# Kernel tuning notes

Measured on AMD Instinct MI355X. Metric: run time of the kernel, lower is better.

## Reference

```python
import jax, jax.numpy as jnp
import numpy as np

N_NODES = 100000
N_EDGES = 1600000
IN_CH = 64
HID = 64
OUT_CH = 128
EDGE_CH = 3
OBS_RANGE = 0.5
ATK_RANGE = 0.3


def setup_inputs() -> dict:
    key = jax.random.key(0)
    k = jax.random.split(key, 8)
    # node features: first column is an integer node type in {0,1,2}
    node_type = jax.random.randint(k[0], (N_NODES, 1), 0, 3).astype(jnp.float32)
    feats = jax.random.normal(k[1], (N_NODES, IN_CH - 1), dtype=jnp.float32)
    x = jnp.concatenate([node_type, feats], axis=-1)
    edge_index = jax.random.randint(k[2], (2, N_EDGES), 0, N_NODES)
    # edge_attr[:,0] = distance in [0,1)
    edge_attr = jax.random.uniform(k[3], (N_EDGES, EDGE_CH), dtype=jnp.float32)
    s1 = 1.0 / np.sqrt(2 * IN_CH + EDGE_CH)
    s2 = 1.0 / np.sqrt(HID)
    W1 = jax.random.normal(k[4], (2 * IN_CH + EDGE_CH, HID), dtype=jnp.float32) * s1
    b1 = jnp.zeros((HID,), dtype=jnp.float32)
    W2 = jax.random.normal(k[5], (HID, OUT_CH), dtype=jnp.float32) * s2
    b2 = jnp.zeros((OUT_CH,), dtype=jnp.float32)
    return {"x": x, "edge_index": edge_index, "edge_attr": edge_attr,
            "W1": W1, "b1": b1, "W2": W2, "b2": b2}


def reference(x, edge_index, edge_attr, W1, b1, W2, b2):
    src = edge_index[0]  # j (source)
    dst = edge_index[1]  # i (target)
    x_j = x[src]         # [E, IN_CH]
    x_i = x[dst]         # [E, IN_CH]
    h = jnp.concatenate([x_i, x_j, edge_attr], axis=-1)  # [E, 2*IN_CH+3]
    msg = jax.nn.relu(h @ W1 + b1) @ W2 + b2             # [E, OUT_CH]
    dist = edge_attr[:, 0]
    ntype = x_j[:, 0]
    mask = jnp.where(ntype == 0, dist < OBS_RANGE,
                     jnp.where(ntype == 1, dist < ATK_RANGE, True))
    msg = mask[:, None].astype(msg.dtype) * msg
    out = jax.ops.segment_sum(msg, dst, num_segments=x.shape[0])  # [N, OUT_CH]
    return jax.nn.relu(out)
```

## Files before the change

### kernel.cpp

```cpp
#include <hip/hip_runtime.h>

#define N_NODES 100000
#define N_EDGES 1600000
#define IN_CH   64
#define HID_CH  64
#define OUT_CH  128
#define TILE    128
#define N_TILES (N_EDGES / TILE)

typedef __attribute__((ext_vector_type(8))) __bf16    bf16x8;
typedef __attribute__((ext_vector_type(4))) float     f32x4;
typedef __attribute__((ext_vector_type(2))) _Float16  f16x2;
typedef __attribute__((ext_vector_type(8))) _Float16  f16x8;

__device__ __forceinline__ unsigned short f2bf(float f) {
    union { float f; unsigned int i; } c;
    c.f = f;
    unsigned int u = c.i;
    unsigned int r = (u + 0x7FFFu + ((u >> 16) & 1u)) >> 16;
    return (unsigned short)r;
}

__device__ __forceinline__ void atomic_pk_add_f16(unsigned int* addr, f16x2 val) {
    typedef __attribute__((address_space(1))) f16x2 gf16x2;
    __builtin_amdgcn_global_atomic_fadd_v2f16((gf16x2*)(void*)addr, val);
}

__global__ void gnn_prep(const float* __restrict__ xf,
                         unsigned short* __restrict__ xb,
                         unsigned char* __restrict__ ntype,
                         uint4* __restrict__ hz,
                         float4* __restrict__ cz) {
    int i = blockIdx.x * blockDim.x + threadIdx.x;
    if (i < 1600000) {
        float4 v = reinterpret_cast<const float4*>(xf)[i];
        ushort4 o;
        o.x = f2bf(v.x); o.y = f2bf(v.y); o.z = f2bf(v.z); o.w = f2bf(v.w);
        reinterpret_cast<ushort4*>(xb)[i] = o;
        if ((i & 15) == 0) {
            int n = i >> 4;
            ntype[n] = (v.x == 0.0f) ? 0 : ((v.x == 1.0f) ? 1 : 2);
        }
    } else if (i < 2400000) {
        hz[i - 1600000] = (uint4){0u, 0u, 0u, 0u};
    } else if (i < 2425000) {
        cz[i - 2400000] = (float4){0.f, 0.f, 0.f, 0.f};
    }
}

__global__ __launch_bounds__(256, 4) void gnn_edge_hidden(
    const unsigned char*  __restrict__ ntype,
    const unsigned short* __restrict__ xb,
    const int*            __restrict__ eidx,
    const float*          __restrict__ ea,
    const float*          __restrict__ W1,
    const float*          __restrict__ b1,
    unsigned int*         __restrict__ hsum,
    float*                __restrict__ cnt)
{
    __shared__ __align__(16) unsigned short W1T[64][136];
    __shared__ float eas[128][3];
    __shared__ int   dstm[128];
    __shared__ int   srcs[128];

    const int tid  = threadIdx.x;
    const int wave = tid >> 6;
    const int lane = tid & 63;
    const int q    = lane >> 4;
    const int m16  = lane & 15;

    for (int idx = tid; idx < 128 * 64; idx += 256) {
        int k = idx >> 6, n = idx & 63;
        W1T[n][k] = f2bf(W1[idx]);
    }
    if (tid < 64) {
        float4 tl;
        tl.x = W1[128 * 64 + tid];
        tl.y = W1[129 * 64 + tid];
        tl.z = W1[130 * 64 + tid];
        tl.w = b1[tid];
        *reinterpret_cast<float4*>(&W1T[tid][128]) = tl;
    }

    for (int t = blockIdx.x; t < N_TILES; t += gridDim.x) {
        __syncthreads();
        if (tid < 128) {
            int e = t * TILE + tid;
            int s = eidx[e];
            int d = eidx[N_EDGES + e];
            float a0 = ea[e * 3 + 0];
            float a1 = ea[e * 3 + 1];
            float a2 = ea[e * 3 + 2];
            eas[tid][0] = a0; eas[tid][1] = a1; eas[tid][2] = a2;
            int ntc = ntype[s];
            bool mk = (ntc == 0) ? (a0 < 0.5f) : ((ntc == 1) ? (a0 < 0.3f) : true);
            dstm[tid] = mk ? (int)(0x80000000u | (unsigned)d) : 0;
            srcs[tid] = mk ? s : 0;
            if (mk) unsafeAtomicAdd(&cnt[d], 1.0f);
        }
        __syncthreads();

        const int ebase = wave * 32;

        f32x4 acc1[2][4];
#pragma unroll
        for (int mt = 0; mt < 2; ++mt) {
            float e0[4], e1[4], e2[4];
#pragma unroll
            for (int r = 0; r < 4; ++r) {
                int el = ebase + mt * 16 + q * 4 + r;
                e0[r] = eas[el][0]; e1[r] = eas[el][1]; e2[r] = eas[el][2];
            }
#pragma unroll
            for (int nt = 0; nt < 4; ++nt) {
                int n = nt * 16 + m16;
                float4 wt = *reinterpret_cast<const float4*>(&W1T[n][128]);
#pragma unroll
                for (int r = 0; r < 4; ++r)
                    acc1[mt][nt][r] = wt.w + e0[r] * wt.x + e1[r] * wt.y + e2[r] * wt.z;
            }
        }

#pragma unroll
        for (int kc = 0; kc < 4; ++kc) {
            bf16x8 af[2];
#pragma unroll
            for (int mt = 0; mt < 2; ++mt) {
                int el = ebase + mt * 16 + m16;
                int dm = dstm[el];
                int node = (kc < 2) ? (dm & 0x7FFFFFFF) : srcs[el];
                af[mt] = *reinterpret_cast<const bf16x8*>(
                    xb + (size_t)node * IN_CH + (kc & 1) * 32 + q * 8);
            }
#pragma unroll
            for (int nt = 0; nt < 4; ++nt) {
                bf16x8 bfr = *reinterpret_cast<const bf16x8*>(
                    &W1T[nt * 16 + m16][kc * 32 + q * 8]);
                acc1[0][nt] = __builtin_amdgcn_mfma_f32_16x16x32_bf16(af[0], bfr, acc1[0][nt], 0, 0, 0);
                acc1[1][nt] = __builtin_amdgcn_mfma_f32_16x16x32_bf16(af[1], bfr, acc1[1][nt], 0, 0, 0);
            }
        }

#pragma unroll
        for (int mt = 0; mt < 2; ++mt) {
#pragma unroll
            for (int r = 0; r < 4; ++r) {
                int el = ebase + mt * 16 + q * 4 + r;
                int dm = dstm[el];
                if (dm < 0) {
                    unsigned int* hbase = hsum + (size_t)(dm & 0x7FFFFFFF) * 32;
                    float v0 = acc1[mt][0][r]; v0 = v0 > 0.f ? v0 : 0.f;
                    float v1 = acc1[mt][1][r]; v1 = v1 > 0.f ? v1 : 0.f;
                    float v2 = acc1[mt][2][r]; v2 = v2 > 0.f ? v2 : 0.f;
                    float v3 = acc1[mt][3][r]; v3 = v3 > 0.f ? v3 : 0.f;
                    if (v0 + v1 > 0.f) {
                        f16x2 p01 = {(_Float16)v0, (_Float16)v1};
                        atomic_pk_add_f16(hbase + m16, p01);
                    }
                    if (v2 + v3 > 0.f) {
                        f16x2 p23 = {(_Float16)v2, (_Float16)v3};
                        atomic_pk_add_f16(hbase + 16 + m16, p23);
                    }
                }
            }
        }
    }
}

__global__ __launch_bounds__(256, 4) void gnn_node_out(
    const _Float16* __restrict__ hsum,
    const float*    __restrict__ cnt,
    const float*    __restrict__ W2,
    const float*    __restrict__ b2,
    float*          __restrict__ out)
{
    __shared__ __align__(16) unsigned short W2T[128][72];
    __shared__ float b2s[128];

    const int tid  = threadIdx.x;
    const int wave = tid >> 6;
    const int lane = tid & 63;
    const int q    = lane >> 4;
    const int m16  = lane & 15;

    const int nodeBase = (blockIdx.x * 4 + wave) * 32;

    f16x8 hpre[2][2];
    float cc[2][4];
#pragma unroll
    for (int kc = 0; kc < 2; ++kc)
#pragma unroll
        for (int mt = 0; mt < 2; ++mt) {
            int node = nodeBase + mt * 16 + m16;
            if (node >= N_NODES) node = N_NODES - 1;
            hpre[kc][mt] = *reinterpret_cast<const f16x8*>(
                hsum + (size_t)node * HID_CH + kc * 32 + q * 8);
        }
#pragma unroll
    for (int mt = 0; mt < 2; ++mt)
#pragma unroll
        for (int r = 0; r < 4; ++r) {
            int n = nodeBase + mt * 16 + q * 4 + r;
            cc[mt][r] = (n < N_NODES) ? cnt[n] : 0.0f;
        }

    for (int idx = tid; idx < 64 * 128; idx += 256) {
        int p = idx >> 7, n = idx & 127;
        int ch = (p >> 1) + 16 * (p & 1) + ((p >= 32) ? 16 : 0);
        W2T[n][p] = f2bf(W2[ch * 128 + n]);
    }
    if (tid < 128) b2s[tid] = b2[tid];
    __syncthreads();

    if (nodeBase >= N_NODES) return;

    f32x4 acc[2][8];
#pragma unroll
    for (int mt = 0; mt < 2; ++mt)
#pragma unroll
        for (int nt = 0; nt < 8; ++nt)
            acc[mt][nt] = (f32x4){0.0f, 0.0f, 0.0f, 0.0f};

#pragma unroll
    for (int kc = 0; kc < 2; ++kc) {
        bf16x8 af[2];
#pragma unroll
        for (int mt = 0; mt < 2; ++mt) {
            union { bf16x8 v; unsigned short u[8]; } rr;
#pragma unroll
            for (int j = 0; j < 8; ++j) rr.u[j] = f2bf((float)hpre[kc][mt][j]);
            af[mt] = rr.v;
        }
#pragma unroll
        for (int nt = 0; nt < 8; ++nt) {
            bf16x8 bfr = *reinterpret_cast<const bf16x8*>(
                &W2T[nt * 16 + m16][kc * 32 + q * 8]);
            acc[0][nt] = __builtin_amdgcn_mfma_f32_16x16x32_bf16(af[0], bfr, acc[0][nt], 0, 0, 0);
            acc[1][nt] = __builtin_amdgcn_mfma_f32_16x16x32_bf16(af[1], bfr, acc[1][nt], 0, 0, 0);
        }
    }

#pragma unroll
    for (int mt = 0; mt < 2; ++mt) {
        int nn[4];
#pragma unroll
        for (int r = 0; r < 4; ++r)
            nn[r] = nodeBase + mt * 16 + q * 4 + r;
#pragma unroll
        for (int nt = 0; nt < 8; ++nt) {
            int col = nt * 16 + m16;
            float bb = b2s[col];
#pragma unroll
            for (int r = 0; r < 4; ++r) {
                if (nn[r] < N_NODES) {
                    float v = acc[mt][nt][r] + cc[mt][r] * bb;
                    out[(size_t)nn[r] * OUT_CH + col] = v > 0.0f ? v : 0.0f;
                }
            }
        }
    }
}

extern "C" void kernel_launch(void* const* d_in, const int* in_sizes, int n_in,
                              void* d_out, int out_size, void* d_ws, size_t ws_size,
                              hipStream_t stream) {
    const float* x  = (const float*)d_in[0];
    const int*   ei = (const int*)d_in[1];
    const float* ea = (const float*)d_in[2];
    const float* W1 = (const float*)d_in[3];
    const float* b1 = (const float*)d_in[4];
    const float* W2 = (const float*)d_in[5];
    const float* b2 = (const float*)d_in[6];
    float* out = (float*)d_out;

    char* wsb = (char*)d_ws;
    unsigned int*   hsum  = (unsigned int*)wsb;
    float*          cnt   = (float*)(wsb + 12800000);
    unsigned short* xb    = (unsigned short*)(wsb + 13200000);
    unsigned char*  ntype = (unsigned char*)(wsb + 26000000);

    gnn_prep<<<(2425000 + 255) / 256, 256, 0, stream>>>(
        x, xb, ntype, (uint4*)hsum, (float4*)cnt);

    gnn_edge_hidden<<<2048, 256, 0, stream>>>(ntype, xb, ei, ea, W1, b1, hsum, cnt);

    gnn_node_out<<<(N_NODES + 127) / 128, 256, 0, stream>>>(
        (const _Float16*)hsum, cnt, W2, b2, out);
}
```

Before: 271.9 us.

## Sort masked edges by destination via CSR build and reduce in shared memory

Replaces the global fp16 packed atomics on the hidden sum with a counting sort of masked edges by destination: a histogram, a three-kernel scan, and a scatter into packed edge records. Each block then handles 64 destination nodes, accumulates hidden activations in a shared-memory float buffer with run-length merged LDS atomics, and writes hsum once. This removes global atomic contention and the zeroing of hsum, and accumulates in fp32 before the fp16 store. In exchange it adds several launches, an extra pass over the edges, a scatter with global atomics, and 25.6 MB of record traffic. The W2 permutation in the node kernel is simplified to match the new hsum channel layout.

```diff
diff --git a/kernel.cpp b/kernel.cpp
--- a/kernel.cpp
+++ b/kernel.cpp
@@ -6,12 +6,24 @@
 #define HID_CH  64
 #define OUT_CH  128
 #define TILE    128
-#define N_TILES (N_EDGES / TILE)
+#define DPB     64
+#define N_EBLK  ((N_NODES + DPB - 1) / DPB)
+#define N_SCANB ((N_NODES + 255) / 256)
 
 typedef __attribute__((ext_vector_type(8))) __bf16    bf16x8;
 typedef __attribute__((ext_vector_type(4))) float     f32x4;
 typedef __attribute__((ext_vector_type(2))) _Float16  f16x2;
 typedef __attribute__((ext_vector_type(8))) _Float16  f16x8;
+
+#define OFF_HSUM   0
+#define OFF_XB     12800000
+#define OFF_SREC   25600000
+#define OFF_CNT    51200000
+#define OFF_DEG    51600000
+#define OFF_RPTR   52000000
+#define OFF_CUR    52400016
+#define OFF_BSUM   52800016
+#define OFF_NTYPE  52801600
 
 __device__ __forceinline__ unsigned short f2bf(float f) {
     union { float f; unsigned int i; } c;
@@ -21,16 +33,14 @@
     return (unsigned short)r;
 }
 
-__device__ __forceinline__ void atomic_pk_add_f16(unsigned int* addr, f16x2 val) {
-    typedef __attribute__((address_space(1))) f16x2 gf16x2;
-    __builtin_amdgcn_global_atomic_fadd_v2f16((gf16x2*)(void*)addr, val);
+__device__ __forceinline__ bool edge_mask(int ntc, float a0) {
+    return (ntc == 0) ? (a0 < 0.5f) : ((ntc == 1) ? (a0 < 0.3f) : true);
 }
 
 __global__ void gnn_prep(const float* __restrict__ xf,
                          unsigned short* __restrict__ xb,
                          unsigned char* __restrict__ ntype,
-                         uint4* __restrict__ hz,
-                         float4* __restrict__ cz) {
+                         uint4* __restrict__ degz) {
     int i = blockIdx.x * blockDim.x + threadIdx.x;
     if (i < 1600000) {
         float4 v = reinterpret_cast<const float4*>(xf)[i];
@@ -41,27 +51,116 @@
             int n = i >> 4;
             ntype[n] = (v.x == 0.0f) ? 0 : ((v.x == 1.0f) ? 1 : 2);
         }
-    } else if (i < 2400000) {
-        hz[i - 1600000] = (uint4){0u, 0u, 0u, 0u};
-    } else if (i < 2425000) {
-        cz[i - 2400000] = (float4){0.f, 0.f, 0.f, 0.f};
-    }
-}
-
-__global__ __launch_bounds__(256, 4) void gnn_edge_hidden(
-    const unsigned char*  __restrict__ ntype,
+    } else if (i < 1625000) {
+        degz[i - 1600000] = (uint4){0u, 0u, 0u, 0u};
+    }
+}
+
+__global__ void gnn_hist(const int* __restrict__ eidx,
+                         const float* __restrict__ ea,
+                         const unsigned char* __restrict__ ntype,
+                         unsigned int* __restrict__ deg) {
+    int e = blockIdx.x * blockDim.x + threadIdx.x;
+    if (e < N_EDGES) {
+        int s = eidx[e];
+        float a0 = ea[e * 3];
+        if (edge_mask(ntype[s], a0))
+            atomicAdd(deg + eidx[N_EDGES + e], 1u);
+    }
+}
+
+__global__ void gnn_scan_a(const unsigned int* __restrict__ deg,
+                           unsigned int* __restrict__ rptr,
+                           unsigned int* __restrict__ bsum,
+                           float* __restrict__ cnt) {
+    __shared__ unsigned int sd[256];
+    int t = threadIdx.x;
+    int i = blockIdx.x * 256 + t;
+    unsigned v = (i < N_NODES) ? deg[i] : 0u;
+    sd[t] = v;
+    __syncthreads();
+    for (int off = 1; off < 256; off <<= 1) {
+        unsigned x = (t >= off) ? sd[t - off] : 0u;
+        __syncthreads();
+        sd[t] += x;
+        __syncthreads();
+    }
+    unsigned incl = sd[t];
+    if (i < N_NODES) {
+        rptr[i] = incl - v;
+        cnt[i]  = (float)v;
+    }
+    if (t == 255) bsum[blockIdx.x] = incl;
+}
+
+__global__ void gnn_scan_b(unsigned int* __restrict__ bsum,
+                           unsigned int* __restrict__ rptr) {
+    __shared__ unsigned int sd[512];
+    int t = threadIdx.x;
+    unsigned v = (t < N_SCANB) ? bsum[t] : 0u;
+    sd[t] = v;
+    __syncthreads();
+    for (int off = 1; off < 512; off <<= 1) {
+        unsigned x = (t >= off) ? sd[t - off] : 0u;
+        __syncthreads();
+        sd[t] += x;
+        __syncthreads();
+    }
+    if (t < N_SCANB) bsum[t] = sd[t] - v;
+    if (t == 511) rptr[N_NODES] = sd[511];
+}
+
+__global__ void gnn_scan_c(unsigned int* __restrict__ rptr,
+                           const unsigned int* __restrict__ bsum,
+                           unsigned int* __restrict__ cur) {
+    int i = blockIdx.x * 256 + threadIdx.x;
+    if (i < N_NODES) {
+        unsigned r = rptr[i] + bsum[blockIdx.x];
+        rptr[i] = r;
+        cur[i]  = r;
+    }
+}
+
+__global__ void gnn_scatter(const int* __restrict__ eidx,
+                            const float* __restrict__ ea,
+                            const unsigned char* __restrict__ ntype,
+                            unsigned int* __restrict__ cur,
+                            float4* __restrict__ srec) {
+    int e = blockIdx.x * blockDim.x + threadIdx.x;
+    if (e < N_EDGES) {
+        int s = eidx[e];
+        float a0 = ea[e * 3 + 0];
+        if (edge_mask(ntype[s], a0)) {
+            int d = eidx[N_EDGES + e];
+            float a1 = ea[e * 3 + 1];
+            float a2 = ea[e * 3 + 2];
+            unsigned pos = atomicAdd(cur + d, 1u);
+            union { f16x2 v; float f; } pk;
+            pk.v = (f16x2){(_Float16)a1, (_Float16)a2};
+            float4 rec;
+            rec.x = __int_as_float(s);
+            rec.y = __int_as_float(d);
+            rec.z = a0;
+            rec.w = pk.f;
+            srec[pos] = rec;
+        }
+    }
+}
+
+__global__ __launch_bounds__(256, 4) void gnn_edge_sorted(
     const unsigned short* __restrict__ xb,
-    const int*            __restrict__ eidx,
-    const float*          __restrict__ ea,
+    const float4*         __restrict__ srec,
+    const unsigned int*   __restrict__ rptr,
     const float*          __restrict__ W1,
     const float*          __restrict__ b1,
-    unsigned int*         __restrict__ hsum,
-    float*                __restrict__ cnt)
+    unsigned int*         __restrict__ hsum)
 {
     __shared__ __align__(16) unsigned short W1T[64][136];
+    __shared__ float accum[65][64];
     __shared__ float eas[128][3];
-    __shared__ int   dstm[128];
     __shared__ int   srcs[128];
+    __shared__ int   dstg[128];
+    __shared__ int   dstl[128];
 
     const int tid  = threadIdx.x;
     const int wave = tid >> 6;
@@ -81,26 +180,35 @@
         tl.w = b1[tid];
         *reinterpret_cast<float4*>(&W1T[tid][128]) = tl;
     }
-
-    for (int t = blockIdx.x; t < N_TILES; t += gridDim.x) {
-        __syncthreads();
-        if (tid < 128) {
-            int e = t * TILE + tid;
-            int s = eidx[e];
-            int d = eidx[N_EDGES + e];
-            float a0 = ea[e * 3 + 0];
-            float a1 = ea[e * 3 + 1];
-            float a2 = ea[e * 3 + 2];
-            eas[tid][0] = a0; eas[tid][1] = a1; eas[tid][2] = a2;
-            int ntc = ntype[s];
-            bool mk = (ntc == 0) ? (a0 < 0.5f) : ((ntc == 1) ? (a0 < 0.3f) : true);
-            dstm[tid] = mk ? (int)(0x80000000u | (unsigned)d) : 0;
-            srcs[tid] = mk ? s : 0;
-            if (mk) unsafeAtomicAdd(&cnt[d], 1.0f);
-        }
-        __syncthreads();
-
-        const int ebase = wave * 32;
+    for (int idx = tid; idx < 65 * 64; idx += 256)
+        (&accum[0][0])[idx] = 0.0f;
+
+    const int base = blockIdx.x * DPB;
+    const int dEnd = (base + DPB < N_NODES) ? base + DPB : N_NODES;
+    const unsigned eStart = rptr[base];
+    const unsigned eEnd   = rptr[dEnd];
+    __syncthreads();
+
+    const int ebase = wave * 32;
+
+    for (unsigned t0 = eStart; t0 < eEnd; t0 += TILE) {
+        int cntE = (int)(eEnd - t0); if (cntE > TILE) cntE = TILE;
+        if (tid < TILE) {
+            if (tid < cntE) {
+                float4 rec = srec[t0 + tid];
+                int s = __float_as_int(rec.x);
+                int d = __float_as_int(rec.y);
+                srcs[tid] = s; dstg[tid] = d; dstl[tid] = d - base;
+                union { float f; f16x2 v; } pk; pk.f = rec.w;
+                eas[tid][0] = rec.z;
+                eas[tid][1] = (float)pk.v[0];
+                eas[tid][2] = (float)pk.v[1];
+            } else {
+                srcs[tid] = 0; dstg[tid] = 0; dstl[tid] = 64;
+                eas[tid][0] = 0.f; eas[tid][1] = 0.f; eas[tid][2] = 0.f;
+            }
+        }
+        __syncthreads();
 
         f32x4 acc1[2][4];
 #pragma unroll
@@ -127,8 +235,7 @@
 #pragma unroll
             for (int mt = 0; mt < 2; ++mt) {
                 int el = ebase + mt * 16 + m16;
-                int dm = dstm[el];
-                int node = (kc < 2) ? (dm & 0x7FFFFFFF) : srcs[el];
+                int node = (kc < 2) ? dstg[el] : srcs[el];
                 af[mt] = *reinterpret_cast<const bf16x8*>(
                     xb + (size_t)node * IN_CH + (kc & 1) * 32 + q * 8);
             }
@@ -143,26 +250,36 @@
 
 #pragma unroll
         for (int mt = 0; mt < 2; ++mt) {
-#pragma unroll
-            for (int r = 0; r < 4; ++r) {
-                int el = ebase + mt * 16 + q * 4 + r;
-                int dm = dstm[el];
-                if (dm < 0) {
-                    unsigned int* hbase = hsum + (size_t)(dm & 0x7FFFFFFF) * 32;
-                    float v0 = acc1[mt][0][r]; v0 = v0 > 0.f ? v0 : 0.f;
-                    float v1 = acc1[mt][1][r]; v1 = v1 > 0.f ? v1 : 0.f;
-                    float v2 = acc1[mt][2][r]; v2 = v2 > 0.f ? v2 : 0.f;
-                    float v3 = acc1[mt][3][r]; v3 = v3 > 0.f ? v3 : 0.f;
-                    if (v0 + v1 > 0.f) {
-                        f16x2 p01 = {(_Float16)v0, (_Float16)v1};
-                        atomic_pk_add_f16(hbase + m16, p01);
-                    }
-                    if (v2 + v3 > 0.f) {
-                        f16x2 p23 = {(_Float16)v2, (_Float16)v3};
-                        atomic_pk_add_f16(hbase + 16 + m16, p23);
-                    }
-                }
-            }
+            int rowb = ebase + mt * 16 + q * 4;
+            int d0 = dstl[rowb + 0];
+            int d1 = dstl[rowb + 1];
+            int d2 = dstl[rowb + 2];
+            int d3 = dstl[rowb + 3];
+#pragma unroll
+            for (int nt = 0; nt < 4; ++nt) {
+                int ch = nt * 16 + m16;
+                float v0 = acc1[mt][nt][0]; v0 = v0 > 0.f ? v0 : 0.f;
+                float v1 = acc1[mt][nt][1]; v1 = v1 > 0.f ? v1 : 0.f;
+                float v2 = acc1[mt][nt][2]; v2 = v2 > 0.f ? v2 : 0.f;
+                float v3 = acc1[mt][nt][3]; v3 = v3 > 0.f ? v3 : 0.f;
+                float s = v0; int cur = d0;
+                if (d1 == cur) s += v1; else { atomicAdd(&accum[cur][ch], s); s = v1; cur = d1; }
+                if (d2 == cur) s += v2; else { atomicAdd(&accum[cur][ch], s); s = v2; cur = d2; }
+                if (d3 == cur) s += v3; else { atomicAdd(&accum[cur][ch], s); s = v3; cur = d3; }
+                atomicAdd(&accum[cur][ch], s);
+            }
+        }
+        __syncthreads();
+    }
+
+    for (int idx = tid; idx < DPB * 32; idx += 256) {
+        int d = idx >> 5;
+        int c = idx & 31;
+        int gd = base + d;
+        if (gd < N_NODES) {
+            union { f16x2 v; unsigned u; } pk;
+            pk.v = (f16x2){(_Float16)accum[d][2 * c], (_Float16)accum[d][2 * c + 1]};
+            hsum[(size_t)gd * 32 + c] = pk.u;
         }
     }
 }
@@ -205,9 +322,8 @@
         }
 
     for (int idx = tid; idx < 64 * 128; idx += 256) {
-        int p = idx >> 7, n = idx & 127;
-        int ch = (p >> 1) + 16 * (p & 1) + ((p >= 32) ? 16 : 0);
-        W2T[n][p] = f2bf(W2[ch * 128 + n]);
+        int k = idx >> 7, n = idx & 127;
+        W2T[n][k] = f2bf(W2[k * 128 + n]);
     }
     if (tid < 128) b2s[tid] = b2[tid];
     __syncthreads();
@@ -274,16 +390,23 @@
     float* out = (float*)d_out;
 
     char* wsb = (char*)d_ws;
-    unsigned int*   hsum  = (unsigned int*)wsb;
-    float*          cnt   = (float*)(wsb + 12800000);
-    unsigned short* xb    = (unsigned short*)(wsb + 13200000);
-    unsigned char*  ntype = (unsigned char*)(wsb + 26000000);
-
-    gnn_prep<<<(2425000 + 255) / 256, 256, 0, stream>>>(
-        x, xb, ntype, (uint4*)hsum, (float4*)cnt);
-
-    gnn_edge_hidden<<<2048, 256, 0, stream>>>(ntype, xb, ei, ea, W1, b1, hsum, cnt);
-
+    unsigned int*   hsum  = (unsigned int*)  (wsb + OFF_HSUM);
+    unsigned short* xb    = (unsigned short*)(wsb + OFF_XB);
+    float4*         srec  = (float4*)        (wsb + OFF_SREC);
+    float*          cnt   = (float*)         (wsb + OFF_CNT);
+    unsigned int*   deg   = (unsigned int*)  (wsb + OFF_DEG);
+    unsigned int*   rptr  = (unsigned int*)  (wsb + OFF_RPTR);
+    unsigned int*   curp  = (unsigned int*)  (wsb + OFF_CUR);
+    unsigned int*   bsum  = (unsigned int*)  (wsb + OFF_BSUM);
+    unsigned char*  ntype = (unsigned char*) (wsb + OFF_NTYPE);
+
+    gnn_prep<<<(1625000 + 255) / 256, 256, 0, stream>>>(x, xb, ntype, (uint4*)deg);
+    gnn_hist<<<N_EDGES / 256, 256, 0, stream>>>(ei, ea, ntype, deg);
+    gnn_scan_a<<<N_SCANB, 256, 0, stream>>>(deg, rptr, bsum, cnt);
+    gnn_scan_b<<<1, 512, 0, stream>>>(bsum, rptr);
+    gnn_scan_c<<<N_SCANB, 256, 0, stream>>>(rptr, bsum, curp);
+    gnn_scatter<<<N_EDGES / 256, 256, 0, stream>>>(ei, ea, ntype, curp, srec);
+    gnn_edge_sorted<<<N_EBLK, 256, 0, stream>>>(xb, srec, rptr, W1, b1, hsum);
     gnn_node_out<<<(N_NODES + 127) / 128, 256, 0, stream>>>(
         (const _Float16*)hsum, cnt, W2, b2, out);
 }
```

New measurement: 369.6 us. 1.36x slower.

## Precompute per-node W1 projections and reduce edge stage to gather-add-relu

Applied to the files above, without the earlier changes.

Splits the first-layer GEMM by linearity: a new node-level kernel computes x@W1_dst and x@W1_src once per node into an fp16 buffer z. The per-edge kernel then only gathers two 64-channel rows of z, adds the edge-attribute and bias term, applies relu and scatters with packed fp16 atomics, using four threads per edge. Masked edges are skipped early, before the destination and the other attributes are loaded. This removes per-edge MFMA work and x gathers in exchange for an extra 25.6MB z buffer with its write and random reads. It also adds fp16 rounding of the pre-activation and changes the hsum channel ordering, so W2T is now transposed without the previous permutation.

```diff
diff --git a/kernel.cpp b/kernel.cpp
--- a/kernel.cpp
+++ b/kernel.cpp
@@ -5,13 +5,17 @@
 #define IN_CH   64
 #define HID_CH  64
 #define OUT_CH  128
-#define TILE    128
-#define N_TILES (N_EDGES / TILE)
 
 typedef __attribute__((ext_vector_type(8))) __bf16    bf16x8;
 typedef __attribute__((ext_vector_type(4))) float     f32x4;
 typedef __attribute__((ext_vector_type(2))) _Float16  f16x2;
 typedef __attribute__((ext_vector_type(8))) _Float16  f16x8;
+
+#define OFF_HSUM   0
+#define OFF_XB     12800000
+#define OFF_Z      25600000
+#define OFF_CNT    51200000
+#define OFF_NTYPE  51600000
 
 __device__ __forceinline__ unsigned short f2bf(float f) {
     union { float f; unsigned int i; } c;
@@ -48,20 +52,12 @@
     }
 }
 
-__global__ __launch_bounds__(256, 4) void gnn_edge_hidden(
-    const unsigned char*  __restrict__ ntype,
+__global__ __launch_bounds__(256, 4) void gnn_zgemm(
     const unsigned short* __restrict__ xb,
-    const int*            __restrict__ eidx,
-    const float*          __restrict__ ea,
     const float*          __restrict__ W1,
-    const float*          __restrict__ b1,
-    unsigned int*         __restrict__ hsum,
-    float*                __restrict__ cnt)
+    _Float16*             __restrict__ z)
 {
-    __shared__ __align__(16) unsigned short W1T[64][136];
-    __shared__ float eas[128][3];
-    __shared__ int   dstm[128];
-    __shared__ int   srcs[128];
+    __shared__ __align__(16) unsigned short BT[128][72];
 
     const int tid  = threadIdx.x;
     const int wave = tid >> 6;
@@ -69,98 +65,120 @@
     const int q    = lane >> 4;
     const int m16  = lane & 15;
 
-    for (int idx = tid; idx < 128 * 64; idx += 256) {
-        int k = idx >> 6, n = idx & 63;
-        W1T[n][k] = f2bf(W1[idx]);
-    }
+    for (int idx = tid; idx < 64 * 128; idx += 256) {
+        int k = idx >> 7, j = idx & 127;
+        BT[j][k] = f2bf(W1[(k + ((j >= 64) ? 64 : 0)) * 64 + (j & 63)]);
+    }
+    __syncthreads();
+
+    const int nodeBase = (blockIdx.x * 4 + wave) * 32;
+    if (nodeBase >= N_NODES) return;
+
+    f32x4 acc[2][8];
+#pragma unroll
+    for (int mt = 0; mt < 2; ++mt)
+#pragma unroll
+        for (int nt = 0; nt < 8; ++nt)
+            acc[mt][nt] = (f32x4){0.0f, 0.0f, 0.0f, 0.0f};
+
+#pragma unroll
+    for (int kc = 0; kc < 2; ++kc) {
+        bf16x8 af[2];
+#pragma unroll
+        for (int mt = 0; mt < 2; ++mt) {
+            int node = nodeBase + mt * 16 + m16;
+            if (node >= N_NODES) node = N_NODES - 1;
+            af[mt] = *reinterpret_cast<const bf16x8*>(
+                xb + (size_t)node * IN_CH + kc * 32 + q * 8);
+        }
+#pragma unroll
+        for (int nt = 0; nt < 8; ++nt) {
+            bf16x8 bfr = *reinterpret_cast<const bf16x8*>(
+                &BT[nt * 16 + m16][kc * 32 + q * 8]);
+            acc[0][nt] = __builtin_amdgcn_mfma_f32_16x16x32_bf16(af[0], bfr, acc[0][nt], 0, 0, 0);
+            acc[1][nt] = __builtin_amdgcn_mfma_f32_16x16x32_bf16(af[1], bfr, acc[1][nt], 0, 0, 0);
+        }
+    }
+
+#pragma unroll
+    for (int mt = 0; mt < 2; ++mt) {
+#pragma unroll
+        for (int nt = 0; nt < 8; ++nt) {
+            int col = nt * 16 + m16;
+#pragma unroll
+            for (int r = 0; r < 4; ++r) {
+                int n = nodeBase + mt * 16 + q * 4 + r;
+                if (n < N_NODES)
+                    z[(size_t)n * 128 + col] = (_Float16)acc[mt][nt][r];
+            }
+        }
+    }
+}
+
+__global__ __launch_bounds__(256, 4) void gnn_edge_lite(
+    const int*           __restrict__ eidx,
+    const float*         __restrict__ ea,
+    const unsigned char* __restrict__ ntype,
+    const _Float16*      __restrict__ z,
+    const float*         __restrict__ W1,
+    const float*         __restrict__ b1,
+    unsigned int*        __restrict__ hsum,
+    float*               __restrict__ cnt)
+{
+    __shared__ __align__(16) float tail[64][4];
+    const int tid = threadIdx.x;
     if (tid < 64) {
         float4 tl;
         tl.x = W1[128 * 64 + tid];
         tl.y = W1[129 * 64 + tid];
         tl.z = W1[130 * 64 + tid];
         tl.w = b1[tid];
-        *reinterpret_cast<float4*>(&W1T[tid][128]) = tl;
-    }
-
-    for (int t = blockIdx.x; t < N_TILES; t += gridDim.x) {
-        __syncthreads();
-        if (tid < 128) {
-            int e = t * TILE + tid;
-            int s = eidx[e];
-            int d = eidx[N_EDGES + e];
-            float a0 = ea[e * 3 + 0];
-            float a1 = ea[e * 3 + 1];
-            float a2 = ea[e * 3 + 2];
-            eas[tid][0] = a0; eas[tid][1] = a1; eas[tid][2] = a2;
-            int ntc = ntype[s];
-            bool mk = (ntc == 0) ? (a0 < 0.5f) : ((ntc == 1) ? (a0 < 0.3f) : true);
-            dstm[tid] = mk ? (int)(0x80000000u | (unsigned)d) : 0;
-            srcs[tid] = mk ? s : 0;
-            if (mk) unsafeAtomicAdd(&cnt[d], 1.0f);
-        }
-        __syncthreads();
-
-        const int ebase = wave * 32;
-
-        f32x4 acc1[2][4];
-#pragma unroll
-        for (int mt = 0; mt < 2; ++mt) {
-            float e0[4], e1[4], e2[4];
-#pragma unroll
-            for (int r = 0; r < 4; ++r) {
-                int el = ebase + mt * 16 + q * 4 + r;
-                e0[r] = eas[el][0]; e1[r] = eas[el][1]; e2[r] = eas[el][2];
-            }
-#pragma unroll
-            for (int nt = 0; nt < 4; ++nt) {
-                int n = nt * 16 + m16;
-                float4 wt = *reinterpret_cast<const float4*>(&W1T[n][128]);
-#pragma unroll
-                for (int r = 0; r < 4; ++r)
-                    acc1[mt][nt][r] = wt.w + e0[r] * wt.x + e1[r] * wt.y + e2[r] * wt.z;
-            }
-        }
-
-#pragma unroll
-        for (int kc = 0; kc < 4; ++kc) {
-            bf16x8 af[2];
-#pragma unroll
-            for (int mt = 0; mt < 2; ++mt) {
-                int el = ebase + mt * 16 + m16;
-                int dm = dstm[el];
-                int node = (kc < 2) ? (dm & 0x7FFFFFFF) : srcs[el];
-                af[mt] = *reinterpret_cast<const bf16x8*>(
-                    xb + (size_t)node * IN_CH + (kc & 1) * 32 + q * 8);
-            }
-#pragma unroll
-            for (int nt = 0; nt < 4; ++nt) {
-                bf16x8 bfr = *reinterpret_cast<const bf16x8*>(
-                    &W1T[nt * 16 + m16][kc * 32 + q * 8]);
-                acc1[0][nt] = __builtin_amdgcn_mfma_f32_16x16x32_bf16(af[0], bfr, acc1[0][nt], 0, 0, 0);
-                acc1[1][nt] = __builtin_amdgcn_mfma_f32_16x16x32_bf16(af[1], bfr, acc1[1][nt], 0, 0, 0);
-            }
-        }
-
-#pragma unroll
-        for (int mt = 0; mt < 2; ++mt) {
-#pragma unroll
-            for (int r = 0; r < 4; ++r) {
-                int el = ebase + mt * 16 + q * 4 + r;
-                int dm = dstm[el];
-                if (dm < 0) {
-                    unsigned int* hbase = hsum + (size_t)(dm & 0x7FFFFFFF) * 32;
-                    float v0 = acc1[mt][0][r]; v0 = v0 > 0.f ? v0 : 0.f;
-                    float v1 = acc1[mt][1][r]; v1 = v1 > 0.f ? v1 : 0.f;
-                    float v2 = acc1[mt][2][r]; v2 = v2 > 0.f ? v2 : 0.f;
-                    float v3 = acc1[mt][3][r]; v3 = v3 > 0.f ? v3 : 0.f;
-                    if (v0 + v1 > 0.f) {
-                        f16x2 p01 = {(_Float16)v0, (_Float16)v1};
-                        atomic_pk_add_f16(hbase + m16, p01);
-                    }
-                    if (v2 + v3 > 0.f) {
-                        f16x2 p23 = {(_Float16)v2, (_Float16)v3};
-                        atomic_pk_add_f16(hbase + 16 + m16, p23);
-                    }
+        *reinterpret_cast<float4*>(tail[tid]) = tl;
+    }
+    __syncthreads();
+
+    const int gid    = blockIdx.x * 256 + tid;
+    const int p      = gid & 3;
+    const int stride = (gridDim.x * 256) >> 2;
+
+    for (int e = gid >> 2; e < N_EDGES; e += stride) {
+        int   s  = eidx[e];
+        float a0 = ea[e * 3 + 0];
+        int ntc = ntype[s];
+        bool mk = (ntc == 0) ? (a0 < 0.5f) : ((ntc == 1) ? (a0 < 0.3f) : true);
+        if (!mk) continue;
+
+        int   d  = eidx[N_EDGES + e];
+        float a1 = ea[e * 3 + 1];
+        float a2 = ea[e * 3 + 2];
+        if (p == 0) unsafeAtomicAdd(&cnt[d], 1.0f);
+
+        const _Float16* zdp = z + (size_t)d * 128 + p * 16;
+        const _Float16* zsp = z + (size_t)s * 128 + 64 + p * 16;
+        f16x8 zd0 = *reinterpret_cast<const f16x8*>(zdp);
+        f16x8 zd1 = *reinterpret_cast<const f16x8*>(zdp + 8);
+        f16x8 zs0 = *reinterpret_cast<const f16x8*>(zsp);
+        f16x8 zs1 = *reinterpret_cast<const f16x8*>(zsp + 8);
+
+        unsigned int* hb = hsum + (size_t)d * 32 + p * 8;
+#pragma unroll
+        for (int half = 0; half < 2; ++half) {
+            f16x8 zd = half ? zd1 : zd0;
+            f16x8 zs = half ? zs1 : zs0;
+#pragma unroll
+            for (int jj = 0; jj < 4; ++jj) {
+                int ch = p * 16 + half * 8 + 2 * jj;
+                float4 wA = *reinterpret_cast<const float4*>(tail[ch]);
+                float4 wB = *reinterpret_cast<const float4*>(tail[ch + 1]);
+                float h0 = (float)zd[2 * jj]     + (float)zs[2 * jj]
+                         + wA.w + a0 * wA.x + a1 * wA.y + a2 * wA.z;
+                float h1 = (float)zd[2 * jj + 1] + (float)zs[2 * jj + 1]
+                         + wB.w + a0 * wB.x + a1 * wB.y + a2 * wB.z;
+                h0 = h0 > 0.f ? h0 : 0.f;
+                h1 = h1 > 0.f ? h1 : 0.f;
+                if (h0 + h1 > 0.f) {
+                    f16x2 pk = {(_Float16)h0, (_Float16)h1};
+                    atomic_pk_add_f16(hb + half * 4 + jj, pk);
                 }
             }
         }
@@ -205,9 +223,8 @@
         }
 
     for (int idx = tid; idx < 64 * 128; idx += 256) {
-        int p = idx >> 7, n = idx & 127;
-        int ch = (p >> 1) + 16 * (p & 1) + ((p >= 32) ? 16 : 0);
-        W2T[n][p] = f2bf(W2[ch * 128 + n]);
+        int k = idx >> 7, n = idx & 127;
+        W2T[n][k] = f2bf(W2[k * 128 + n]);
     }
     if (tid < 128) b2s[tid] = b2[tid];
     __syncthreads();
@@ -274,15 +291,18 @@
     float* out = (float*)d_out;
 
     char* wsb = (char*)d_ws;
-    unsigned int*   hsum  = (unsigned int*)wsb;
-    float*          cnt   = (float*)(wsb + 12800000);
-    unsigned short* xb    = (unsigned short*)(wsb + 13200000);
-    unsigned char*  ntype = (unsigned char*)(wsb + 26000000);
+    unsigned int*   hsum  = (unsigned int*)  (wsb + OFF_HSUM);
+    unsigned short* xb    = (unsigned short*)(wsb + OFF_XB);
+    _Float16*       z     = (_Float16*)      (wsb + OFF_Z);
+    float*          cnt   = (float*)         (wsb + OFF_CNT);
+    unsigned char*  ntype = (unsigned char*) (wsb + OFF_NTYPE);
 
     gnn_prep<<<(2425000 + 255) / 256, 256, 0, stream>>>(
         x, xb, ntype, (uint4*)hsum, (float4*)cnt);
 
-    gnn_edge_hidden<<<2048, 256, 0, stream>>>(ntype, xb, ei, ea, W1, b1, hsum, cnt);
+    gnn_zgemm<<<(N_NODES + 127) / 128, 256, 0, stream>>>(xb, W1, z);
+
+    gnn_edge_lite<<<2048, 256, 0, stream>>>(ei, ea, ntype, z, W1, b1, hsum, cnt);
 
     gnn_node_out<<<(N_NODES + 127) / 128, 256, 0, stream>>>(
         (const _Float16*)hsum, cnt, W2, b2, out);
```

Result: slower. 918.2 us (+237.7%).
